# Performance work log

Measured on AMD Instinct MI355X. Metric: run time of the kernel, lower is better.

The kernel has to match this reference:

```python
import jax, jax.numpy as jnp
import numpy as np

TEMPERATURE = 0.5
W_WITHIN = 1.0
W_CROSS = 0.5
MARGIN = 0.1


def setup_inputs() -> dict:
    key = jax.random.key(0)
    k1, k2 = jax.random.split(key)
    features = jax.random.normal(k1, (8192, 256), dtype=jnp.float32)
    gene_labels = jax.random.randint(k2, (8192,), 0, 200, dtype=jnp.int64 if jax.config.jax_enable_x64 else jnp.int32)
    return {"features": features, "gene_labels": gene_labels}


def reference(features, gene_labels):
    B = features.shape[0]
    # L2-normalize rows, full pairwise cosine similarity / temperature
    fn = features / jnp.linalg.norm(features, axis=1, keepdims=True)
    sim = (fn @ fn.T) / TEMPERATURE  # [B, B]

    same = gene_labels[:, None] == gene_labels[None, :]  # [B, B]
    eye = jnp.eye(B, dtype=bool)
    same_off = same & ~eye            # same-gene, off-diagonal (gene_similarity)
    neg = ~same                       # different-gene pairs (cross_gene_mask)
    has_neg = neg.any(axis=1)

    # Per-anchor logsumexp over negatives (sim of anchor i to all different-gene samples)
    neg_sim = jnp.where(neg, sim, -jnp.inf)
    lse_neg = jax.scipy.special.logsumexp(neg_sim, axis=1)
    lse_neg = jnp.where(has_neg, lse_neg, 0.0)  # rows with no negatives are masked out below

    # Within-gene loss: for each unordered same-gene pair (i<j) with gene != -1 and
    # anchor i having >=1 negative: CE([sim_ij, neg_sims_i], label=0)
    #   = -sim_ij + logaddexp(sim_ij, lse_neg_i) = softplus(lse_neg_i - sim_ij)
    upper = jnp.triu(jnp.ones((B, B), dtype=bool), k=1)
    valid_gene = (gene_labels != -1)[:, None]
    pair_mask = same_off & upper & valid_gene & has_neg[:, None]
    within_gene_loss = jnp.where(pair_mask, jax.nn.softplus(lse_neg[:, None] - sim), 0.0).sum()

    # Cross-gene loss: mean over all ordered different-gene pairs of relu(sim - margin)
    cross_cnt = neg.sum()
    cross_sum = jnp.where(neg, jax.nn.relu(sim - MARGIN), 0.0).sum()
    cross_gene_loss = jnp.where(cross_cnt > 0, cross_sum / jnp.maximum(cross_cnt, 1).astype(sim.dtype), 0.0)

    total_loss = W_WITHIN * within_gene_loss + W_CROSS * cross_gene_loss
    num_within_gene_pairs = same_off.sum().astype(sim.dtype)
    num_cross_gene_pairs = cross_cnt
    return total_loss, within_gene_loss, cross_gene_loss, num_within_gene_pairs, num_cross_gene_pairs
```

## Files before the change

### kernel.cpp

```cpp
#include <hip/hip_runtime.h>
#include <math.h>

#define B_N   8192
#define D_K   256
#define NGENE 200
#define MAXN  512

typedef short  bf16x8 __attribute__((ext_vector_type(8)));
typedef float  f32x4  __attribute__((ext_vector_type(4)));

#define OFF_FNBF    0u
#define OFF_LPART   4194304u
#define OFF_HIST    4718592u
#define OFF_OFFS    4719616u
#define OFF_SORTED  4720640u
#define OFF_CROSSP  4753408u
#define OFF_WITHINP 4755456u
#define OFF_CCORR   4756480u
#define OFF_DONE    4757504u

__device__ __forceinline__ unsigned short f2bf(float f) {
    unsigned int u = __float_as_uint(f);
    unsigned int r = u + 0x7fffu + ((u >> 16) & 1u);
    return (unsigned short)(r >> 16);
}
__device__ __forceinline__ float bf2f_lo(unsigned int u) { return __uint_as_float(u << 16); }
__device__ __forceinline__ float bf2f_hi(unsigned int u) { return __uint_as_float(u & 0xffff0000u); }

__global__ __launch_bounds__(256) void k_prep(const float* __restrict__ feat,
                                              const int* __restrict__ lab,
                                              unsigned short* __restrict__ fnbf,
                                              int* __restrict__ hist,
                                              int* __restrict__ offs,
                                              int* __restrict__ sorted,
                                              int* __restrict__ done) {
    int b = blockIdx.x;
    if (b < 2048) {
        int wave = threadIdx.x >> 6, lane = threadIdx.x & 63;
        int row  = b * 4 + wave;
        const float4* src = reinterpret_cast<const float4*>(feat + (size_t)row * D_K);
        float4 v = src[lane];
        float ss = v.x * v.x + v.y * v.y + v.z * v.z + v.w * v.w;
#pragma unroll
        for (int m = 1; m < 64; m <<= 1) ss += __shfl_xor(ss, m);
        float rn = 1.0f / sqrtf(ss);
        ushort4 o;
        o.x = f2bf(v.x * rn); o.y = f2bf(v.y * rn);
        o.z = f2bf(v.z * rn); o.w = f2bf(v.w * rn);
        reinterpret_cast<ushort4*>(fnbf + (size_t)row * D_K)[lane] = o;
        return;
    }
    int g = b - 2048, t = threadIdx.x;
    __shared__ int sc[256];
    if (g == 0 && t == 0) *done = 0;

    int r0 = t * 32, lt = 0, eq = 0;
    for (int r = r0; r < r0 + 32; ++r) {
        int lb = lab[r];
        lt += (lb >= 0 && lb < g) ? 1 : 0;
        eq += (lb == g) ? 1 : 0;
    }
    sc[t] = lt;
    __syncthreads();
#pragma unroll
    for (int d = 128; d > 0; d >>= 1) {
        if (t < d) sc[t] += sc[t + d];
        __syncthreads();
    }
    int start = sc[0];
    __syncthreads();
    sc[t] = eq;
    __syncthreads();
#pragma unroll
    for (int d = 1; d < 256; d <<= 1) {
        int x = (t >= d) ? sc[t - d] : 0;
        __syncthreads();
        sc[t] += x;
        __syncthreads();
    }
    int w = start + sc[t] - eq;
    for (int r = r0; r < r0 + 32; ++r)
        if (lab[r] == g) sorted[w++] = r;
    if (t == 0)   offs[g] = start;
    if (t == 255) hist[g] = sc[255];
}

#define GLOAD8(arr, vo) do {                                                                   \
    asm volatile("global_load_dwordx4 %0, %1, %2 offset:0"   : "=v"(arr[0]) : "v"(vo), "s"(fb)); \
    asm volatile("global_load_dwordx4 %0, %1, %2 offset:64"  : "=v"(arr[1]) : "v"(vo), "s"(fb)); \
    asm volatile("global_load_dwordx4 %0, %1, %2 offset:128" : "=v"(arr[2]) : "v"(vo), "s"(fb)); \
    asm volatile("global_load_dwordx4 %0, %1, %2 offset:192" : "=v"(arr[3]) : "v"(vo), "s"(fb)); \
    asm volatile("global_load_dwordx4 %0, %1, %2 offset:256" : "=v"(arr[4]) : "v"(vo), "s"(fb)); \
    asm volatile("global_load_dwordx4 %0, %1, %2 offset:320" : "=v"(arr[5]) : "v"(vo), "s"(fb)); \
    asm volatile("global_load_dwordx4 %0, %1, %2 offset:384" : "=v"(arr[6]) : "v"(vo), "s"(fb)); \
    asm volatile("global_load_dwordx4 %0, %1, %2 offset:448" : "=v"(arr[7]) : "v"(vo), "s"(fb)); \
} while (0)

#define GL_LDS16(gp, lp)                                                          \
    __builtin_amdgcn_global_load_lds(                                             \
        (const __attribute__((address_space(1))) unsigned int*)(gp),              \
        (__attribute__((address_space(3))) unsigned int*)(lp), 16, 0, 0)

#define Z4 ((f32x4){0.f, 0.f, 0.f, 0.f})
#define MFMA(A, B, C) __builtin_amdgcn_mfma_f32_16x16x32_bf16(A, B, C, 0, 0, 0)

#define EPI(AC, LS, CS) do {                                    \
    _Pragma("unroll")                                           \
    for (int r = 0; r < 4; ++r) {                               \
        float av = AC[r];                                       \
        LS[r] += __expf(2.0f * av);                             \
        CS += fmaxf(av - 0.05f, 0.f);                           \
    }                                                           \
} while (0)

#define WAIT_VM(n) do { asm volatile("s_waitcnt vmcnt(" #n ")" ::: "memory"); \
                        __builtin_amdgcn_sched_barrier(0); } while (0)

#define WAIT_LGKM0 do { asm volatile("s_waitcnt lgkmcnt(0)" ::: "memory"); \
                        __builtin_amdgcn_sched_barrier(0); } while (0)

#define STAGE_W(BOFF, T) do {                                                      \
    const char* gt = gw + (unsigned)(T) * 8192u;                                   \
    _Pragma("unroll")                                                              \
    for (int q = 0; q < 8; ++q)                                                    \
        GL_LDS16(gt + sv[q], smem_c + wbase + (BOFF) + q * 1024u);                 \
} while (0)

__global__ __launch_bounds__(256, 2) void k_pairwise(const unsigned short* __restrict__ fnbf,
                                                     float* __restrict__ l_part,
                                                     float* __restrict__ cross_part) {
    __shared__ __align__(16) char smem_c[65536];
    __shared__ float shc[4];

    int tid = threadIdx.x;
    int wave = tid >> 6, lane = tid & 63;
    int g16 = lane >> 4, l16 = lane & 15;
    int l7 = l16 & 7;
    int rg = blockIdx.x, cwin = blockIdx.y;
    int r0 = rg * 256 + wave * 64;
    const unsigned short* fb = fnbf;
    unsigned wbase = (unsigned)wave * 16384u;

    bf16x8 a0[8], a1[8], a2[8], a3[8];
    unsigned voa = (unsigned)(r0 + l16) * 512u + (unsigned)g16 * 16u;
    GLOAD8(a0, voa); voa += 8192u;
    GLOAD8(a1, voa); voa += 8192u;
    GLOAD8(a2, voa); voa += 8192u;
    GLOAD8(a3, voa);

    const char* gw = (const char*)fnbf + (size_t)cwin * 262144u;
    unsigned sv[8];
#pragma unroll
    for (int q = 0; q < 8; ++q) {
        int f = q * 64 + lane;
        int col = f >> 5;
        sv[q] = (unsigned)(col * 512 + (((lane & 31) ^ (col & 7)) << 4));
    }

    STAGE_W(0u, 0);
    STAGE_W(8192u, 1);
    WAIT_VM(16);

    float lsum[4][4] = {};
    float cs0 = 0.f, cs1 = 0.f, cs2 = 0.f, cs3 = 0.f;
    int vb = l16 * 512;

#pragma unroll 1
    for (int st = 0; st < 32; ++st) {
        if (st < 31) { WAIT_VM(8); }
        else         { WAIT_VM(0); }

        const char* base = smem_c + wbase + (unsigned)((st & 1) << 13);
        f32x4 acc0 = Z4, acc1 = Z4, acc2 = Z4, acc3 = Z4;
#pragma unroll
        for (int ks = 0; ks < 8; ++ks) {
            const char* p = base + (unsigned)(vb + ((((ks << 2) | g16) ^ l7) << 4));
            bf16x8 bv = *(const bf16x8*)p;
            acc0 = MFMA(a0[ks], bv, acc0);
            acc1 = MFMA(a1[ks], bv, acc1);
            acc2 = MFMA(a2[ks], bv, acc2);
            acc3 = MFMA(a3[ks], bv, acc3);
        }
        EPI(acc0, lsum[0], cs0); EPI(acc1, lsum[1], cs1);
        EPI(acc2, lsum[2], cs2); EPI(acc3, lsum[3], cs3);

        if (st < 30) {
            WAIT_LGKM0;
            STAGE_W((unsigned)((st & 1) << 13), st + 2);
        }
    }

#pragma unroll
    for (int t = 0; t < 4; ++t)
#pragma unroll
        for (int r = 0; r < 4; ++r) {
            float v = lsum[t][r];
            v += __shfl_xor(v, 1); v += __shfl_xor(v, 2);
            v += __shfl_xor(v, 4); v += __shfl_xor(v, 8);
            if (l16 == 0)
                l_part[(size_t)cwin * B_N + r0 + t * 16 + g16 * 4 + r] = v;
        }

    float c = (cs0 + cs1) + (cs2 + cs3);
#pragma unroll
    for (int m = 1; m < 64; m <<= 1) c += __shfl_xor(c, m);
    if (lane == 0) shc[wave] = c;
    __syncthreads();
    if (tid == 0)
        cross_part[cwin * 32 + rg] = shc[0] + shc[1] + shc[2] + shc[3];
}

__device__ __forceinline__ float dot_g(const uint4* __restrict__ fu, int i, int j) {
    const uint4* pa = fu + (size_t)i * 32;
    const uint4* pb = fu + (size_t)j * 32;
    float d = 0.f;
#pragma unroll
    for (int k = 0; k < 32; ++k) {
        uint4 ua = pa[k], ub = pb[k];
        d = fmaf(bf2f_lo(ua.x), bf2f_lo(ub.x), d);
        d = fmaf(bf2f_hi(ua.x), bf2f_hi(ub.x), d);
        d = fmaf(bf2f_lo(ua.y), bf2f_lo(ub.y), d);
        d = fmaf(bf2f_hi(ua.y), bf2f_hi(ub.y), d);
        d = fmaf(bf2f_lo(ua.z), bf2f_lo(ub.z), d);
        d = fmaf(bf2f_hi(ua.z), bf2f_hi(ub.z), d);
        d = fmaf(bf2f_lo(ua.w), bf2f_lo(ub.w), d);
        d = fmaf(bf2f_hi(ua.w), bf2f_hi(ub.w), d);
    }
    return d;
}

__global__ __launch_bounds__(256) void k_within(const unsigned short* __restrict__ fnbf,
                                                const int* __restrict__ hist,
                                                const int* __restrict__ offs,
                                                const int* __restrict__ sorted,
                                                const float* __restrict__ l_part,
                                                const float* __restrict__ cross_part,
                                                float* __restrict__ within_part,
                                                float* __restrict__ cross_corr,
                                                int* __restrict__ done,
                                                float* __restrict__ out) {
    int g = blockIdx.x;
    int n = hist[g], start = offs[g];
    int t = threadIdx.x;
    int wave = t >> 6, lane = t & 63;
    int g16 = lane >> 4, l16 = lane & 15;

    __shared__ float sim[128 * 130];
    __shared__ int   rid[MAXN];
    __shared__ float slse[MAXN];
    __shared__ float red[256];
    __shared__ int   is_last;

    for (int idx = t; idx < n; idx += 256) rid[idx] = sorted[start + idx];
    __syncthreads();

    float ccor = 0.f, wsum = 0.f;

    if (n <= 128) {
        int NT = (n + 15) >> 4;
        const bf16x8* fv = reinterpret_cast<const bf16x8*>(fnbf);
        for (int tile = wave; tile < NT * NT; tile += 4) {
            int ti = tile / NT, tj = tile - ti * NT;
            int ia = ti * 16 + l16;
            int ib = tj * 16 + l16;
            int ra = rid[ia < n ? ia : (n - 1)];
            int rb = rid[ib < n ? ib : (n - 1)];
            f32x4 acc = Z4;
#pragma unroll
            for (int ks = 0; ks < 8; ++ks) {
                bf16x8 av = fv[(size_t)ra * 32 + ks * 4 + g16];
                bf16x8 bv = fv[(size_t)rb * 32 + ks * 4 + g16];
                acc = MFMA(av, bv, acc);
            }
            int si = ti * 16 + g16 * 4;
            int sj = tj * 16 + l16;
#pragma unroll
            for (int r = 0; r < 4; ++r)
                sim[(si + r) * 130 + sj] = acc[r];
        }
        __syncthreads();

        for (int i = t; i < n; i += 256) {
            float raw = 0.f;
#pragma unroll
            for (int k = 0; k < 16; ++k) raw += l_part[(size_t)k * B_N + rid[i]];
            const float* srow = &sim[i * 130];
            float esum = 0.f;
            for (int j = 0; j < n; ++j) {
                float s = 2.0f * srow[j];
                esum += __expf(s);
                ccor += fmaxf(s - 0.1f, 0.f);
            }
            slse[i] = __logf(raw - esum);
        }
        __syncthreads();

        int nn = n * n;
        for (int p = t; p < nn; p += 256) {
            int i = p / n, j = p - i * n;
            if (j <= i) continue;
            float s = 2.0f * sim[i * 130 + j];
            int ai = (rid[i] < rid[j]) ? i : j;
            float x = slse[ai] - s;
            wsum += fmaxf(x, 0.f) + log1pf(__expf(-fabsf(x)));
        }
    } else {
        const uint4* fu = reinterpret_cast<const uint4*>(fnbf);
        for (int i = t; i < n; i += 256) {
            float raw = 0.f;
#pragma unroll
            for (int k = 0; k < 16; ++k) raw += l_part[(size_t)k * B_N + rid[i]];
            float esum = 0.f;
            for (int j = 0; j < n; ++j) {
                float s = 2.0f * dot_g(fu, rid[i], rid[j]);
                esum += __expf(s);
                ccor += fmaxf(s - 0.1f, 0.f);
            }
            slse[i] = __logf(raw - esum);
        }
        __syncthreads();
        int nn = n * n;
        for (int p = t; p < nn; p += 256) {
            int i = p / n, j = p - i * n;
            if (j <= i) continue;
            float s = 2.0f * dot_g(fu, rid[i], rid[j]);
            int ai = (rid[i] < rid[j]) ? i : j;
            float x = slse[ai] - s;
            wsum += fmaxf(x, 0.f) + log1pf(__expf(-fabsf(x)));
        }
    }

    red[t] = wsum;
    __syncthreads();
#pragma unroll
    for (int d2 = 128; d2 > 0; d2 >>= 1) {
        if (t < d2) red[t] += red[t + d2];
        __syncthreads();
    }
    if (t == 0) within_part[g] = red[0];
    __syncthreads();
    red[t] = ccor;
    __syncthreads();
#pragma unroll
    for (int d2 = 128; d2 > 0; d2 >>= 1) {
        if (t < d2) red[t] += red[t + d2];
        __syncthreads();
    }
    if (t == 0) cross_corr[g] = red[0];

    __syncthreads();
    if (t == 0) {
        __threadfence();
        int prev = atomicAdd(done, 1);
        is_last = (prev == NGENE - 1) ? 1 : 0;
    }
    __syncthreads();
    if (!is_last) return;
    __threadfence();

    float cs = 0.f;
    for (int i = t; i < 512; i += 256) cs += cross_part[i];
    float wv = 0.f, cc = 0.f;
    long long s2 = 0;
    if (t < NGENE) {
        wv = within_part[t];
        cc = cross_corr[t];
        long long h = hist[t];
        s2 = h * h;
    }
    float* shc = sim;
    float* shw = sim + 256;
    float* shk = sim + 512;
    long long* shs = reinterpret_cast<long long*>(sim + 768);
    shc[t] = cs; shw[t] = wv; shk[t] = cc; shs[t] = s2;
    __syncthreads();
#pragma unroll
    for (int d = 128; d > 0; d >>= 1) {
        if (t < d) {
            shc[t] += shc[t + d]; shw[t] += shw[t + d];
            shk[t] += shk[t + d]; shs[t] += shs[t + d];
        }
        __syncthreads();
    }
    if (t == 0) {
        long long S  = shs[0];
        long long nw = S - (long long)B_N;
        long long nc = (long long)B_N * (long long)B_N - S;
        float cross_total = 2.0f * shc[0] - shk[0];
        float cross_loss = (nc > 0) ? (cross_total / (float)(nc > 1 ? nc : 1)) : 0.f;
        float within     = shw[0];
        out[0] = within + 0.5f * cross_loss;
        out[1] = within;
        out[2] = cross_loss;
        out[3] = (float)nw;
        out[4] = (float)nc;
    }
}

extern "C" void kernel_launch(void* const* d_in, const int* in_sizes, int n_in,
                              void* d_out, int out_size, void* d_ws, size_t ws_size,
                              hipStream_t stream) {
    const float* feat = (const float*)d_in[0];
    const int*   lab  = (const int*)d_in[1];
    float* out = (float*)d_out;
    char* ws = (char*)d_ws;

    unsigned short* fnbf = (unsigned short*)(ws + OFF_FNBF);
    float* l_part        = (float*)(ws + OFF_LPART);
    int*   hist          = (int*)(ws + OFF_HIST);
    int*   offs          = (int*)(ws + OFF_OFFS);
    int*   sorted        = (int*)(ws + OFF_SORTED);
    float* cross_part    = (float*)(ws + OFF_CROSSP);
    float* within_part   = (float*)(ws + OFF_WITHINP);
    float* cross_corr    = (float*)(ws + OFF_CCORR);
    int*   done          = (int*)(ws + OFF_DONE);

    k_prep<<<2048 + NGENE, 256, 0, stream>>>(feat, lab, fnbf, hist, offs, sorted, done);
    k_pairwise<<<dim3(32, 16), 256, 0, stream>>>(fnbf, l_part, cross_part);
    k_within<<<NGENE, 256, 0, stream>>>(fnbf, hist, offs, sorted, l_part, cross_part,
                                        within_part, cross_corr, done, out);
}
```

Measured before the change: 85.11 us.

## Split pairwise kernel into MFMA producer waves and epilogue consumer waves

Launches 512-thread blocks where four waves compute the MFMA tiles and write accumulators to a double-buffered LDS area, and four other waves compute the exp and relu epilogue from the previous step. This is meant to overlap the transcendental epilogue with matrix math. It adds a block-wide barrier every step, an LDS round-trip for the accumulators, and much larger shared memory per block, which may reduce blocks per CU.

Result: slower. 95.20 us (+11.9%).

```diff
diff --git a/kernel.cpp b/kernel.cpp
--- a/kernel.cpp
+++ b/kernel.cpp
@@ -104,15 +104,6 @@
 #define Z4 ((f32x4){0.f, 0.f, 0.f, 0.f})
 #define MFMA(A, B, C) __builtin_amdgcn_mfma_f32_16x16x32_bf16(A, B, C, 0, 0, 0)
 
-#define EPI(AC, LS, CS) do {                                    \
-    _Pragma("unroll")                                           \
-    for (int r = 0; r < 4; ++r) {                               \
-        float av = AC[r];                                       \
-        LS[r] += __expf(2.0f * av);                             \
-        CS += fmaxf(av - 0.05f, 0.f);                           \
-    }                                                           \
-} while (0)
-
 #define WAIT_VM(n) do { asm volatile("s_waitcnt vmcnt(" #n ")" ::: "memory"); \
                         __builtin_amdgcn_sched_barrier(0); } while (0)
 
@@ -126,85 +117,100 @@
         GL_LDS16(gt + sv[q], smem_c + wbase + (BOFF) + q * 1024u);                 \
 } while (0)
 
-__global__ __launch_bounds__(256, 2) void k_pairwise(const unsigned short* __restrict__ fnbf,
+__global__ __launch_bounds__(512, 2) void k_pairwise(const unsigned short* __restrict__ fnbf,
                                                      float* __restrict__ l_part,
                                                      float* __restrict__ cross_part) {
-    __shared__ __align__(16) char smem_c[65536];
-    __shared__ float shc[4];
+    __shared__ __align__(16) char smem_c[100368];
+    float* shc = (float*)(smem_c + 100352);
 
     int tid = threadIdx.x;
-    int wave = tid >> 6, lane = tid & 63;
+    int w = tid >> 6, lane = tid & 63;
     int g16 = lane >> 4, l16 = lane & 15;
     int l7 = l16 & 7;
     int rg = blockIdx.x, cwin = blockIdx.y;
-    int r0 = rg * 256 + wave * 64;
     const unsigned short* fb = fnbf;
-    unsigned wbase = (unsigned)wave * 16384u;
 
     bf16x8 a0[8], a1[8], a2[8], a3[8];
-    unsigned voa = (unsigned)(r0 + l16) * 512u + (unsigned)g16 * 16u;
-    GLOAD8(a0, voa); voa += 8192u;
-    GLOAD8(a1, voa); voa += 8192u;
-    GLOAD8(a2, voa); voa += 8192u;
-    GLOAD8(a3, voa);
-
     const char* gw = (const char*)fnbf + (size_t)cwin * 262144u;
+    unsigned wbase = (unsigned)w * 16384u;
     unsigned sv[8];
-#pragma unroll
-    for (int q = 0; q < 8; ++q) {
-        int f = q * 64 + lane;
-        int col = f >> 5;
-        sv[q] = (unsigned)(col * 512 + (((lane & 31) ^ (col & 7)) << 4));
-    }
-
-    STAGE_W(0u, 0);
-    STAGE_W(8192u, 1);
-    WAIT_VM(16);
-
-    float lsum[4][4] = {};
-    float cs0 = 0.f, cs1 = 0.f, cs2 = 0.f, cs3 = 0.f;
     int vb = l16 * 512;
 
+    if (w < 4) {
+        int r0 = rg * 256 + w * 64;
+        unsigned voa = (unsigned)(r0 + l16) * 512u + (unsigned)g16 * 16u;
+        GLOAD8(a0, voa); voa += 8192u;
+        GLOAD8(a1, voa); voa += 8192u;
+        GLOAD8(a2, voa); voa += 8192u;
+        GLOAD8(a3, voa);
+#pragma unroll
+        for (int q = 0; q < 8; ++q) {
+            int f = q * 64 + lane;
+            int col = f >> 5;
+            sv[q] = (unsigned)(col * 512 + (((lane & 31) ^ (col & 7)) << 4));
+        }
+        STAGE_W(0u, 0);
+        STAGE_W(8192u, 1);
+    }
+
+    float lsum1 = 0.f, csum = 0.f;
+
 #pragma unroll 1
-    for (int st = 0; st < 32; ++st) {
-        if (st < 31) { WAIT_VM(8); }
-        else         { WAIT_VM(0); }
-
-        const char* base = smem_c + wbase + (unsigned)((st & 1) << 13);
-        f32x4 acc0 = Z4, acc1 = Z4, acc2 = Z4, acc3 = Z4;
-#pragma unroll
-        for (int ks = 0; ks < 8; ++ks) {
-            const char* p = base + (unsigned)(vb + ((((ks << 2) | g16) ^ l7) << 4));
-            bf16x8 bv = *(const bf16x8*)p;
-            acc0 = MFMA(a0[ks], bv, acc0);
-            acc1 = MFMA(a1[ks], bv, acc1);
-            acc2 = MFMA(a2[ks], bv, acc2);
-            acc3 = MFMA(a3[ks], bv, acc3);
-        }
-        EPI(acc0, lsum[0], cs0); EPI(acc1, lsum[1], cs1);
-        EPI(acc2, lsum[2], cs2); EPI(acc3, lsum[3], cs3);
-
-        if (st < 30) {
-            WAIT_LGKM0;
-            STAGE_W((unsigned)((st & 1) << 13), st + 2);
-        }
-    }
-
-#pragma unroll
-    for (int t = 0; t < 4; ++t)
-#pragma unroll
-        for (int r = 0; r < 4; ++r) {
-            float v = lsum[t][r];
-            v += __shfl_xor(v, 1); v += __shfl_xor(v, 2);
-            v += __shfl_xor(v, 4); v += __shfl_xor(v, 8);
-            if (l16 == 0)
-                l_part[(size_t)cwin * B_N + r0 + t * 16 + g16 * 4 + r] = v;
-        }
-
-    float c = (cs0 + cs1) + (cs2 + cs3);
-#pragma unroll
-    for (int m = 1; m < 64; m <<= 1) c += __shfl_xor(c, m);
-    if (lane == 0) shc[wave] = c;
+    for (int st = 0; st <= 32; ++st) {
+        asm volatile("s_waitcnt lgkmcnt(0)" ::: "memory");
+        __builtin_amdgcn_s_barrier();
+
+        if (w < 4) {
+            if (st < 32) {
+                if (st < 31) { WAIT_VM(8); }
+                else         { WAIT_VM(0); }
+
+                const char* bbase = smem_c + wbase + (unsigned)((st & 1) << 13);
+                f32x4 acc0 = Z4, acc1 = Z4, acc2 = Z4, acc3 = Z4;
+#pragma unroll
+                for (int ks = 0; ks < 8; ++ks) {
+                    const char* p = bbase + (unsigned)(vb + ((((ks << 2) | g16) ^ l7) << 4));
+                    bf16x8 bv = *(const bf16x8*)p;
+                    acc0 = MFMA(a0[ks], bv, acc0);
+                    acc1 = MFMA(a1[ks], bv, acc1);
+                    acc2 = MFMA(a2[ks], bv, acc2);
+                    acc3 = MFMA(a3[ks], bv, acc3);
+                }
+                float* accW = (float*)(smem_c + 65536u + (unsigned)((st & 1) * 17408) +
+                                       (unsigned)w * 4352u);
+                float* pw0 = accW + l16 * 68 + g16 * 4;
+                *(f32x4*)(pw0)      = acc0;
+                *(f32x4*)(pw0 + 16) = acc1;
+                *(f32x4*)(pw0 + 32) = acc2;
+                *(f32x4*)(pw0 + 48) = acc3;
+
+                if (st < 30) {
+                    WAIT_LGKM0;
+                    STAGE_W((unsigned)((st & 1) << 13), st + 2);
+                }
+            }
+        } else if (st >= 1) {
+            const float* accR = (const float*)(smem_c + 65536u +
+                                 (unsigned)(((st - 1) & 1) * 17408) +
+                                 (unsigned)(w - 4) * 4352u);
+#pragma unroll
+            for (int c = 0; c < 16; ++c) {
+                float av = accR[c * 68 + lane];
+                lsum1 += __expf(2.0f * av);
+                csum  += fmaxf(av - 0.05f, 0.f);
+            }
+        }
+    }
+
+    __syncthreads();
+
+    if (w >= 4) {
+        l_part[(size_t)cwin * B_N + rg * 256 + (w - 4) * 64 + lane] = lsum1;
+        float c = csum;
+#pragma unroll
+        for (int m = 1; m < 64; m <<= 1) c += __shfl_xor(c, m);
+        if (lane == 0) shc[w - 4] = c;
+    }
     __syncthreads();
     if (tid == 0)
         cross_part[cwin * 32 + rg] = shc[0] + shc[1] + shc[2] + shc[3];
@@ -416,7 +422,7 @@
     int*   done          = (int*)(ws + OFF_DONE);
 
     k_prep<<<2048 + NGENE, 256, 0, stream>>>(feat, lab, fnbf, hist, offs, sorted, done);
-    k_pairwise<<<dim3(32, 16), 256, 0, stream>>>(fnbf, l_part, cross_part);
+    k_pairwise<<<dim3(32, 16), 512, 0, stream>>>(fnbf, l_part, cross_part);
     k_within<<<NGENE, 256, 0, stream>>>(fnbf, hist, offs, sorted, l_part, cross_part,
                                         within_part, cross_corr, done, out);
 }
```
